# Kernel tuning notes

Measured on AMD Instinct MI355X. Metric: run time of the kernel, lower is better.

The kernel has to match this reference:

```python
import jax, jax.numpy as jnp
import numpy as np

N_CLASS = 32
SOS = 30
EOS = 31
NEG = -10000.0


def setup_inputs() -> dict:
    key = jax.random.key(0)
    k1, k2 = jax.random.split(key)
    seq_len, batch = 512, 2048
    feats = jax.random.normal(k1, (seq_len, batch, N_CLASS), dtype=jnp.float32)
    mask = jnp.ones((seq_len, batch), dtype=jnp.float32)
    transition = jax.random.normal(k2, (N_CLASS, N_CLASS), dtype=jnp.float32)
    # reset_parameters: transitions into <SOS> and out of <EOS> are forbidden
    transition = transition.at[SOS, :].set(NEG)
    transition = transition.at[:, EOS].set(NEG)
    return {"feats": feats, "mask": mask, "transition": transition}


def reference(feats, mask, transition):
    seq_len, batch, n_class = feats.shape
    alpha0 = jnp.full((batch, n_class), NEG, dtype=feats.dtype).at[:, SOS].set(0.0)

    def step(alpha, inp):
        feat, mask_t = inp  # feat: (B, C), mask_t: (B,)
        # scores[b, next, prev] = alpha[b, prev] + transition[next, prev] + feat[b, next]
        scores = alpha[:, None, :] + transition[None, :, :] + feat[:, :, None]
        new_alpha = jax.nn.logsumexp(scores, axis=-1)
        m = mask_t[:, None]
        alpha = new_alpha * m + alpha * (1.0 - m)
        return alpha, None

    alpha, _ = jax.lax.scan(step, alpha0, (feats, mask))
    alpha = alpha + transition[EOS][None, :]
    return jax.nn.logsumexp(alpha, axis=-1)  # (batch,)
```

## Files before the change

kernel.cpp:

```cpp
#include <hip/hip_runtime.h>

#define NCLS  32
#define SOS   30
#define EOS   31
#define LOG2E 1.4426950408889634f
#define LN2   0.6931471805599453f

typedef __attribute__((ext_vector_type(8))) short short8;
typedef __attribute__((ext_vector_type(4))) float f32x4;

__device__ __forceinline__ uint32_t rne_bf16(float x) {
    uint32_t u = __float_as_uint(x);
    return (u + 0x7fffu + ((u >> 16) & 1u)) >> 16;
}

__global__ __launch_bounds__(128, 2) void crf_fwd(const float* __restrict__ feats,
                                                  const float* __restrict__ mask,
                                                  const float* __restrict__ trans,
                                                  float* __restrict__ out,
                                                  int S, int B) {
    __shared__ float mxs[2][NCLS];
    __shared__ __align__(16) float wsh[2][NCLS];
    __shared__ float wsc[2];

    const int tid  = threadIdx.x;
    const int wid  = tid >> 6;
    const int lane = tid & 63;
    const int q  = lane >> 4;
    const int n0 = lane & 15;
    const int k0 = q * 8;
    const int b  = blockIdx.x * 2 + (n0 & 1);
    const int bb = (b < B) ? b : (B - 1);

    if (lane < NCLS) {
        float mx = -3.4e38f;
        #pragma unroll
        for (int k = 0; k < NCLS; ++k)
            mx = fmaxf(mx, wid ? trans[k * NCLS + lane] : trans[lane * NCLS + k]);
        mxs[wid][lane] = mx * LOG2E;
    }
    __builtin_amdgcn_wave_barrier();
    const float* mx_ = mxs[wid];

    const int c1 = ((n0 >> 2) << 3) | (n0 & 3);
    const int c2 = c1 + 4;
    const float nc1 = mx_[c1], nc2 = mx_[c2];
    union { uint32_t u[4]; short8 s; } a1u, a2u;
    #pragma unroll
    for (int j2 = 0; j2 < 4; ++j2) {
        const int ka = k0 + 2 * j2, kb = ka + 1;
        float f0 = __builtin_amdgcn_exp2f((wid ? trans[ka*NCLS + c1] : trans[c1*NCLS + ka]) * LOG2E - nc1);
        float f1 = __builtin_amdgcn_exp2f((wid ? trans[kb*NCLS + c1] : trans[c1*NCLS + kb]) * LOG2E - nc1);
        a1u.u[j2] = rne_bf16(f0) | (rne_bf16(f1) << 16);
        float g0 = __builtin_amdgcn_exp2f((wid ? trans[ka*NCLS + c2] : trans[c2*NCLS + ka]) * LOG2E - nc2);
        float g1 = __builtin_amdgcn_exp2f((wid ? trans[kb*NCLS + c2] : trans[c2*NCLS + kb]) * LOG2E - nc2);
        a2u.u[j2] = rne_bf16(g0) | (rne_bf16(g1) << 16);
    }
    const short8 a1 = a1u.s, a2 = a2u.s;

    const float mtAx = mx_[k0+0] - 6.f, mtAy = mx_[k0+1] - 6.f;
    const float mtAz = mx_[k0+2] - 6.f, mtAw = mx_[k0+3] - 6.f;
    const float mtBx = mx_[k0+4] - 6.f, mtBy = mx_[k0+5] - 6.f;
    const float mtBz = mx_[k0+6] - 6.f, mtBw = mx_[k0+7] - 6.f;

    float E1x = 0.f, E1y = 0.f, E1z = 0.f, E1w = 0.f;
    float E2x = 0.f, E2y = 0.f, E2z = 0.f, E2w = 0.f;
    if (wid == 0) {
        if (q == 3) E2z = 1.0f;
    } else {
        E1x = __builtin_amdgcn_exp2f(trans[EOS*NCLS + k0+0] * LOG2E - mx_[k0+0]);
        E1y = __builtin_amdgcn_exp2f(trans[EOS*NCLS + k0+1] * LOG2E - mx_[k0+1]);
        E1z = __builtin_amdgcn_exp2f(trans[EOS*NCLS + k0+2] * LOG2E - mx_[k0+2]);
        E1w = __builtin_amdgcn_exp2f(trans[EOS*NCLS + k0+3] * LOG2E - mx_[k0+3]);
        E2x = __builtin_amdgcn_exp2f(trans[EOS*NCLS + k0+4] * LOG2E - mx_[k0+4]);
        E2y = __builtin_amdgcn_exp2f(trans[EOS*NCLS + k0+5] * LOG2E - mx_[k0+5]);
        E2z = __builtin_amdgcn_exp2f(trans[EOS*NCLS + k0+6] * LOG2E - mx_[k0+6]);
        E2w = __builtin_amdgcn_exp2f(trans[EOS*NCLS + k0+7] * LOG2E - mx_[k0+7]);
    }
    float C = 0.f, cnt = 0.f;

    const long long fstep = (long long)B * NCLS;
    const int Hf = (S + 1) >> 1;
    const int H  = wid ? (S - Hf) : Hf;
    const int r0 = wid ? (S - 1) : 0;
    const long long dstep = wid ? -fstep : fstep;
    const long long mstep = wid ? -(long long)B : (long long)B;
    const float* fbase = feats + (long long)r0 * fstep + (long long)bb * NCLS + k0;
    const float* mbase = mask + (long long)r0 * B + bb;

#define LOADSLOT(Rf1, Rf2, Rm, T) {                                          \
        const float* _p = fbase + (long long)(T) * dstep;                    \
        Rf1 = *(const f32x4*)_p;                                             \
        Rf2 = *(const f32x4*)(_p + 4);                                       \
        Rm  = mbase[(long long)(T) * mstep];                                 \
    }

#define CONV(Rf1, Rf2, Rm, Ea, Eb, Md) {                                     \
        Ea.x = __builtin_amdgcn_exp2f(fmaf(Rf1.x, LOG2E, mtAx));             \
        Ea.y = __builtin_amdgcn_exp2f(fmaf(Rf1.y, LOG2E, mtAy));             \
        Ea.z = __builtin_amdgcn_exp2f(fmaf(Rf1.z, LOG2E, mtAz));             \
        Ea.w = __builtin_amdgcn_exp2f(fmaf(Rf1.w, LOG2E, mtAw));             \
        Eb.x = __builtin_amdgcn_exp2f(fmaf(Rf2.x, LOG2E, mtBx));             \
        Eb.y = __builtin_amdgcn_exp2f(fmaf(Rf2.y, LOG2E, mtBy));             \
        Eb.z = __builtin_amdgcn_exp2f(fmaf(Rf2.z, LOG2E, mtBz));             \
        Eb.w = __builtin_amdgcn_exp2f(fmaf(Rf2.w, LOG2E, mtBw));             \
        Md = Rm;                                                             \
    }

#define RENORM_E {                                                           \
        float _Dv = __shfl(E1x, n0, 64);          \
        uint32_t _eb = (__float_as_uint(_Dv) >> 23) & 0xffu;                 \
        C += (float)((int)_eb - 127);                                        \
        float _sc = __uint_as_float((254u - _eb) << 23);                     \
        E1x *= _sc; E1y *= _sc; E1z *= _sc; E1w *= _sc;                      \
        E2x *= _sc; E2y *= _sc; E2z *= _sc; E2w *= _sc;                      \
    }

#define STEPF(EFa, EFb, EM, RN) {                                            \
        uint32_t p0 = __builtin_amdgcn_perm(__float_as_uint(E1y), __float_as_uint(E1x), 0x07060302u); \
        uint32_t p1 = __builtin_amdgcn_perm(__float_as_uint(E1w), __float_as_uint(E1z), 0x07060302u); \
        uint32_t p2 = __builtin_amdgcn_perm(__float_as_uint(E2y), __float_as_uint(E2x), 0x07060302u); \
        uint32_t p3 = __builtin_amdgcn_perm(__float_as_uint(E2w), __float_as_uint(E2z), 0x07060302u); \
        union { uint32_t u[4]; short8 s; } _bu;                              \
        _bu.u[0] = p0; _bu.u[1] = p1; _bu.u[2] = p2; _bu.u[3] = p3;          \
        const f32x4 _z = {0.f, 0.f, 0.f, 0.f};                               \
        f32x4 _d1 = __builtin_amdgcn_mfma_f32_16x16x32_bf16(a1, _bu.s, _z, 0, 0, 0); \
        f32x4 _d2 = __builtin_amdgcn_mfma_f32_16x16x32_bf16(a2, _bu.s, _z, 0, 0, 0); \
        const bool _s = (EM != 0.0f);                                        \
        E1x = _s ? _d1[0] * EFa.x : E1x;  E1y = _s ? _d1[1] * EFa.y : E1y;   \
        E1z = _s ? _d1[2] * EFa.z : E1z;  E1w = _s ? _d1[3] * EFa.w : E1w;   \
        E2x = _s ? _d2[0] * EFb.x : E2x;  E2y = _s ? _d2[1] * EFb.y : E2y;   \
        E2z = _s ? _d2[2] * EFb.z : E2z;  E2w = _s ? _d2[3] * EFb.w : E2w;   \
        cnt += EM;                                                           \
        if (RN) RENORM_E                                                     \
    }

#define STEPB(EFa, EFb, EM, RN) {                                            \
        float t1x = E1x * EFa.x, t1y = E1y * EFa.y, t1z = E1z * EFa.z, t1w = E1w * EFa.w; \
        float t2x = E2x * EFb.x, t2y = E2y * EFb.y, t2z = E2z * EFb.z, t2w = E2w * EFb.w; \
        uint32_t p0 = __builtin_amdgcn_perm(__float_as_uint(t1y), __float_as_uint(t1x), 0x07060302u); \
        uint32_t p1 = __builtin_amdgcn_perm(__float_as_uint(t1w), __float_as_uint(t1z), 0x07060302u); \
        uint32_t p2 = __builtin_amdgcn_perm(__float_as_uint(t2y), __float_as_uint(t2x), 0x07060302u); \
        uint32_t p3 = __builtin_amdgcn_perm(__float_as_uint(t2w), __float_as_uint(t2z), 0x07060302u); \
        union { uint32_t u[4]; short8 s; } _bu;                              \
        _bu.u[0] = p0; _bu.u[1] = p1; _bu.u[2] = p2; _bu.u[3] = p3;          \
        const f32x4 _z = {0.f, 0.f, 0.f, 0.f};                               \
        f32x4 _d1 = __builtin_amdgcn_mfma_f32_16x16x32_bf16(a1, _bu.s, _z, 0, 0, 0); \
        f32x4 _d2 = __builtin_amdgcn_mfma_f32_16x16x32_bf16(a2, _bu.s, _z, 0, 0, 0); \
        const bool _s = (EM != 0.0f);                                        \
        E1x = _s ? _d1[0] : E1x;  E1y = _s ? _d1[1] : E1y;                   \
        E1z = _s ? _d1[2] : E1z;  E1w = _s ? _d1[3] : E1w;                   \
        E2x = _s ? _d2[0] : E2x;  E2y = _s ? _d2[1] : E2y;                   \
        E2z = _s ? _d2[2] : E2z;  E2w = _s ? _d2[3] : E2w;                   \
        cnt += EM;                                                           \
        if (RN) RENORM_E                                                     \
    }

#define PIPELINE(STEPM) {                                                    \
        f32x4 r1_0, r1_1, r1_2, r1_3, r2_0, r2_1, r2_2, r2_3;                \
        float rm_0, rm_1, rm_2, rm_3;                                        \
        f32x4 e1_0, e2_0, e1_1, e2_1;                                        \
        float m_0, m_1;                                                      \
        int tb = 0;                                                          \
        if (H >= 8) {                                                        \
            LOADSLOT(r1_0, r2_0, rm_0, 0); LOADSLOT(r1_1, r2_1, rm_1, 1);    \
            LOADSLOT(r1_2, r2_2, rm_2, 2); LOADSLOT(r1_3, r2_3, rm_3, 3);    \
            CONV(r1_0, r2_0, rm_0, e1_0, e2_0, m_0);                         \
            CONV(r1_1, r2_1, rm_1, e1_1, e2_1, m_1);                         \
            for (; tb + 8 <= H; tb += 4) {                                   \
                STEPM(e1_0, e2_0, m_0, false)                                \
                CONV(r1_2, r2_2, rm_2, e1_0, e2_0, m_0);                     \
                LOADSLOT(r1_0, r2_0, rm_0, tb + 4);                          \
                STEPM(e1_1, e2_1, m_1, false)                                \
                CONV(r1_3, r2_3, rm_3, e1_1, e2_1, m_1);                     \
                LOADSLOT(r1_1, r2_1, rm_1, tb + 5);                          \
                STEPM(e1_0, e2_0, m_0, false)                                \
                CONV(r1_0, r2_0, rm_0, e1_0, e2_0, m_0);                     \
                LOADSLOT(r1_2, r2_2, rm_2, tb + 6);                          \
                STEPM(e1_1, e2_1, m_1, true)                                 \
                CONV(r1_1, r2_1, rm_1, e1_1, e2_1, m_1);                     \
                LOADSLOT(r1_3, r2_3, rm_3, tb + 7);                          \
            }                                                                \
        }                                                                    \
        for (int t = tb; t < H; ++t) {         \
            f32x4 tf1, tf2; float tmr;                                       \
            LOADSLOT(tf1, tf2, tmr, t);                                      \
            f32x4 te1, te2; float tem;                                       \
            CONV(tf1, tf2, tmr, te1, te2, tem);                              \
            STEPM(te1, te2, tem, ((t & 3) == 3))                             \
        }                                                                    \
    }

    if (wid == 0) { PIPELINE(STEPF) } else { PIPELINE(STEPB) }

    if (wid == 1) {
        if (n0 < 2) {
            wsh[n0][k0+0] = E1x * __builtin_amdgcn_exp2f(mx_[k0+0]);
            wsh[n0][k0+1] = E1y * __builtin_amdgcn_exp2f(mx_[k0+1]);
            wsh[n0][k0+2] = E1z * __builtin_amdgcn_exp2f(mx_[k0+2]);
            wsh[n0][k0+3] = E1w * __builtin_amdgcn_exp2f(mx_[k0+3]);
            wsh[n0][k0+4] = E2x * __builtin_amdgcn_exp2f(mx_[k0+4]);
            wsh[n0][k0+5] = E2y * __builtin_amdgcn_exp2f(mx_[k0+5]);
            wsh[n0][k0+6] = E2z * __builtin_amdgcn_exp2f(mx_[k0+6]);
            wsh[n0][k0+7] = E2w * __builtin_amdgcn_exp2f(mx_[k0+7]);
            if (q == 0) wsc[n0] = C + 6.0f * cnt;
        }
    }
    __syncthreads();
    if (wid == 0) {
        const int bc = n0 & 1;
        const f32x4 wa = *(const f32x4*)&wsh[bc][k0];
        const f32x4 wb = *(const f32x4*)&wsh[bc][k0 + 4];
        float dot = E1x * wa.x + E1y * wa.y + E1z * wa.z + E1w * wa.w
                  + E2x * wb.x + E2y * wb.y + E2z * wb.z + E2w * wb.w;
        dot += __shfl_xor(dot, 16, 64);
        dot += __shfl_xor(dot, 32, 64);
        if (q == 0 && n0 < 2 && b < B) {
            out[b] = LN2 * (C + 6.0f * cnt + wsc[bc] + __builtin_amdgcn_logf(dot));
        }
    }
#undef LOADSLOT
#undef CONV
#undef RENORM_E
#undef STEPF
#undef STEPB
#undef PIPELINE
}

extern "C" void kernel_launch(void* const* d_in, const int* in_sizes, int n_in,
                              void* d_out, int out_size, void* d_ws, size_t ws_size,
                              hipStream_t stream) {
    const float* feats = (const float*)d_in[0];
    const float* mask  = (const float*)d_in[1];
    const float* trans = (const float*)d_in[2];
    float* out = (float*)d_out;

    const int B = out_size;
    const int S = in_sizes[1] / B;

    dim3 block(128);
    dim3 grid((B + 1) / 2);
    hipLaunchKernelGGL(crf_fwd, grid, block, 0, stream, feats, mask, trans, out, S, B);
}
```

Baseline: 226.2 us.

## Pack 16 batch columns per MFMA tile and deepen the load pipeline to 8 slots

Each block now handles 16 batch elements, one per MFMA N column, where it used to handle 2 that were replicated across the columns. The grid shrinks by a factor of 8. The prefetch ring grows from 4 to 8 timesteps with an explicit epilogue, and launch bounds drop to 1 block per CU so the extra registers fit. This removes redundant MFMA work and fixed per-block overhead, at the cost of fewer blocks (128 for B=2048) to cover the CUs and lower occupancy for hiding latency.

New measurement: 247.1 us. 9.2% more time.

```diff
diff --git a/kernel.cpp b/kernel.cpp
--- a/kernel.cpp
+++ b/kernel.cpp
@@ -14,14 +14,14 @@
     return (u + 0x7fffu + ((u >> 16) & 1u)) >> 16;
 }
 
-__global__ __launch_bounds__(128, 2) void crf_fwd(const float* __restrict__ feats,
+__global__ __launch_bounds__(128, 1) void crf_fwd(const float* __restrict__ feats,
                                                   const float* __restrict__ mask,
                                                   const float* __restrict__ trans,
                                                   float* __restrict__ out,
                                                   int S, int B) {
     __shared__ float mxs[2][NCLS];
-    __shared__ __align__(16) float wsh[2][NCLS];
-    __shared__ float wsc[2];
+    __shared__ __align__(16) float wsh[16][NCLS];
+    __shared__ float wsc[16];
 
     const int tid  = threadIdx.x;
     const int wid  = tid >> 6;
@@ -29,7 +29,7 @@
     const int q  = lane >> 4;
     const int n0 = lane & 15;
     const int k0 = q * 8;
-    const int b  = blockIdx.x * 2 + (n0 & 1);
+    const int b  = blockIdx.x * 16 + n0;
     const int bb = (b < B) ? b : (B - 1);
 
     if (lane < NCLS) {
@@ -108,7 +108,7 @@
     }
 
 #define RENORM_E {                                                           \
-        float _Dv = __shfl(E1x, n0, 64);          \
+        float _Dv = __shfl(E1x, n0, 64);         \
         uint32_t _eb = (__float_as_uint(_Dv) >> 23) & 0xffu;                 \
         C += (float)((int)_eb - 127);                                        \
         float _sc = __uint_as_float((254u - _eb) << 23);                     \
@@ -157,30 +157,61 @@
     }
 
 #define PIPELINE(STEPM) {                                                    \
-        f32x4 r1_0, r1_1, r1_2, r1_3, r2_0, r2_1, r2_2, r2_3;                \
-        float rm_0, rm_1, rm_2, rm_3;                                        \
+        f32x4 r1_0, r1_1, r1_2, r1_3, r1_4, r1_5, r1_6, r1_7;                \
+        f32x4 r2_0, r2_1, r2_2, r2_3, r2_4, r2_5, r2_6, r2_7;                \
+        float rm_0, rm_1, rm_2, rm_3, rm_4, rm_5, rm_6, rm_7;                \
         f32x4 e1_0, e2_0, e1_1, e2_1;                                        \
         float m_0, m_1;                                                      \
         int tb = 0;                                                          \
-        if (H >= 8) {                                                        \
+        if (H >= 16) {                                                       \
             LOADSLOT(r1_0, r2_0, rm_0, 0); LOADSLOT(r1_1, r2_1, rm_1, 1);    \
             LOADSLOT(r1_2, r2_2, rm_2, 2); LOADSLOT(r1_3, r2_3, rm_3, 3);    \
+            LOADSLOT(r1_4, r2_4, rm_4, 4); LOADSLOT(r1_5, r2_5, rm_5, 5);    \
+            LOADSLOT(r1_6, r2_6, rm_6, 6); LOADSLOT(r1_7, r2_7, rm_7, 7);    \
             CONV(r1_0, r2_0, rm_0, e1_0, e2_0, m_0);                         \
             CONV(r1_1, r2_1, rm_1, e1_1, e2_1, m_1);                         \
-            for (; tb + 8 <= H; tb += 4) {                                   \
+            for (; tb + 16 <= H; tb += 8) {                                  \
                 STEPM(e1_0, e2_0, m_0, false)                                \
                 CONV(r1_2, r2_2, rm_2, e1_0, e2_0, m_0);                     \
-                LOADSLOT(r1_0, r2_0, rm_0, tb + 4);                          \
+                LOADSLOT(r1_0, r2_0, rm_0, tb + 8);                          \
                 STEPM(e1_1, e2_1, m_1, false)                                \
                 CONV(r1_3, r2_3, rm_3, e1_1, e2_1, m_1);                     \
-                LOADSLOT(r1_1, r2_1, rm_1, tb + 5);                          \
+                LOADSLOT(r1_1, r2_1, rm_1, tb + 9);                          \
+                STEPM(e1_0, e2_0, m_0, false)                                \
+                CONV(r1_4, r2_4, rm_4, e1_0, e2_0, m_0);                     \
+                LOADSLOT(r1_2, r2_2, rm_2, tb + 10);                         \
+                STEPM(e1_1, e2_1, m_1, true)                                 \
+                CONV(r1_5, r2_5, rm_5, e1_1, e2_1, m_1);                     \
+                LOADSLOT(r1_3, r2_3, rm_3, tb + 11);                         \
+                STEPM(e1_0, e2_0, m_0, false)                                \
+                CONV(r1_6, r2_6, rm_6, e1_0, e2_0, m_0);                     \
+                LOADSLOT(r1_4, r2_4, rm_4, tb + 12);                         \
+                STEPM(e1_1, e2_1, m_1, false)                                \
+                CONV(r1_7, r2_7, rm_7, e1_1, e2_1, m_1);                     \
+                LOADSLOT(r1_5, r2_5, rm_5, tb + 13);                         \
                 STEPM(e1_0, e2_0, m_0, false)                                \
                 CONV(r1_0, r2_0, rm_0, e1_0, e2_0, m_0);                     \
-                LOADSLOT(r1_2, r2_2, rm_2, tb + 6);                          \
+                LOADSLOT(r1_6, r2_6, rm_6, tb + 14);                         \
                 STEPM(e1_1, e2_1, m_1, true)                                 \
                 CONV(r1_1, r2_1, rm_1, e1_1, e2_1, m_1);                     \
-                LOADSLOT(r1_3, r2_3, rm_3, tb + 7);                          \
+                LOADSLOT(r1_7, r2_7, rm_7, tb + 15);                         \
             }                                                                \
+               \
+            STEPM(e1_0, e2_0, m_0, false)                                    \
+            CONV(r1_2, r2_2, rm_2, e1_0, e2_0, m_0);                         \
+            STEPM(e1_1, e2_1, m_1, false)                                    \
+            CONV(r1_3, r2_3, rm_3, e1_1, e2_1, m_1);                         \
+            STEPM(e1_0, e2_0, m_0, false)                                    \
+            CONV(r1_4, r2_4, rm_4, e1_0, e2_0, m_0);                         \
+            STEPM(e1_1, e2_1, m_1, true)                                     \
+            CONV(r1_5, r2_5, rm_5, e1_1, e2_1, m_1);                         \
+            STEPM(e1_0, e2_0, m_0, false)                                    \
+            CONV(r1_6, r2_6, rm_6, e1_0, e2_0, m_0);                         \
+            STEPM(e1_1, e2_1, m_1, false)                                    \
+            CONV(r1_7, r2_7, rm_7, e1_1, e2_1, m_1);                         \
+            STEPM(e1_0, e2_0, m_0, false)                                    \
+            STEPM(e1_1, e2_1, m_1, true)                                     \
+            tb += 8;                                                         \
         }                                                                    \
         for (int t = tb; t < H; ++t) {         \
             f32x4 tf1, tf2; float tmr;                                       \
@@ -194,29 +225,26 @@
     if (wid == 0) { PIPELINE(STEPF) } else { PIPELINE(STEPB) }
 
     if (wid == 1) {
-        if (n0 < 2) {
-            wsh[n0][k0+0] = E1x * __builtin_amdgcn_exp2f(mx_[k0+0]);
-            wsh[n0][k0+1] = E1y * __builtin_amdgcn_exp2f(mx_[k0+1]);
-            wsh[n0][k0+2] = E1z * __builtin_amdgcn_exp2f(mx_[k0+2]);
-            wsh[n0][k0+3] = E1w * __builtin_amdgcn_exp2f(mx_[k0+3]);
-            wsh[n0][k0+4] = E2x * __builtin_amdgcn_exp2f(mx_[k0+4]);
-            wsh[n0][k0+5] = E2y * __builtin_amdgcn_exp2f(mx_[k0+5]);
-            wsh[n0][k0+6] = E2z * __builtin_amdgcn_exp2f(mx_[k0+6]);
-            wsh[n0][k0+7] = E2w * __builtin_amdgcn_exp2f(mx_[k0+7]);
-            if (q == 0) wsc[n0] = C + 6.0f * cnt;
-        }
+        wsh[n0][k0+0] = E1x * __builtin_amdgcn_exp2f(mx_[k0+0]);
+        wsh[n0][k0+1] = E1y * __builtin_amdgcn_exp2f(mx_[k0+1]);
+        wsh[n0][k0+2] = E1z * __builtin_amdgcn_exp2f(mx_[k0+2]);
+        wsh[n0][k0+3] = E1w * __builtin_amdgcn_exp2f(mx_[k0+3]);
+        wsh[n0][k0+4] = E2x * __builtin_amdgcn_exp2f(mx_[k0+4]);
+        wsh[n0][k0+5] = E2y * __builtin_amdgcn_exp2f(mx_[k0+5]);
+        wsh[n0][k0+6] = E2z * __builtin_amdgcn_exp2f(mx_[k0+6]);
+        wsh[n0][k0+7] = E2w * __builtin_amdgcn_exp2f(mx_[k0+7]);
+        if (q == 0) wsc[n0] = C + 6.0f * cnt;
     }
     __syncthreads();
     if (wid == 0) {
-        const int bc = n0 & 1;
-        const f32x4 wa = *(const f32x4*)&wsh[bc][k0];
-        const f32x4 wb = *(const f32x4*)&wsh[bc][k0 + 4];
+        const f32x4 wa = *(const f32x4*)&wsh[n0][k0];
+        const f32x4 wb = *(const f32x4*)&wsh[n0][k0 + 4];
         float dot = E1x * wa.x + E1y * wa.y + E1z * wa.z + E1w * wa.w
                   + E2x * wb.x + E2y * wb.y + E2z * wb.z + E2w * wb.w;
         dot += __shfl_xor(dot, 16, 64);
         dot += __shfl_xor(dot, 32, 64);
-        if (q == 0 && n0 < 2 && b < B) {
-            out[b] = LN2 * (C + 6.0f * cnt + wsc[bc] + __builtin_amdgcn_logf(dot));
+        if (q == 0 && b < B) {
+            out[b] = LN2 * (C + 6.0f * cnt + wsc[n0] + __builtin_amdgcn_logf(dot));
         }
     }
 #undef LOADSLOT
@@ -239,6 +267,6 @@
     const int S = in_sizes[1] / B;
 
     dim3 block(128);
-    dim3 grid((B + 1) / 2);
+    dim3 grid((B + 15) / 16);
     hipLaunchKernelGGL(crf_fwd, grid, block, 0, stream, feats, mask, trans, out, S, B);
 }
```

## Stage feats and mask through a deep LDS ring via direct global-to-LDS loads

Applied to the files above, without the earlier changes.

Each block now handles 16 batch rows instead of 2, with every MFMA column holding a distinct sequence. Per-step feats and mask slices are prefetched with global_load_lds into a 16-deep per-wave LDS ring, gated by explicit vmcnt waits. The aim is to keep many loads in flight to hide global latency in the serial recurrence and to stop wasting MFMA columns on duplicate batches. In exchange the grid shrinks 8x (128 blocks), occupancy drops to one block per CU with large LDS use, and correctness relies on hand-tuned vmcnt counts.

Result: slower. 313.6 us (+38.6%).

```diff
diff --git a/kernel.cpp b/kernel.cpp
--- a/kernel.cpp
+++ b/kernel.cpp
@@ -6,6 +6,10 @@
 #define LOG2E 1.4426950408889634f
 #define LN2   0.6931471805599453f
 
+#define RING_D  16
+#define SLOT_B  2304
+#define RING_B  (RING_D * SLOT_B)
+
 typedef __attribute__((ext_vector_type(8))) short short8;
 typedef __attribute__((ext_vector_type(4))) float f32x4;
 
@@ -14,14 +18,27 @@
     return (u + 0x7fffu + ((u >> 16) & 1u)) >> 16;
 }
 
-__global__ __launch_bounds__(128, 2) void crf_fwd(const float* __restrict__ feats,
+__device__ __forceinline__ void dma16(const float* g, char* l) {
+    __builtin_amdgcn_global_load_lds((const __attribute__((address_space(1))) void*)g,
+                                     (__attribute__((address_space(3))) void*)l, 16, 0, 0);
+}
+__device__ __forceinline__ void dma4(const float* g, char* l) {
+    __builtin_amdgcn_global_load_lds((const __attribute__((address_space(1))) void*)g,
+                                     (__attribute__((address_space(3))) void*)l, 4, 0, 0);
+}
+
+#define WAITV45 asm volatile("s_waitcnt vmcnt(45)" ::: "memory")
+#define WAITV42 asm volatile("s_waitcnt vmcnt(42)" ::: "memory")
+
+__global__ __launch_bounds__(128, 1) void crf_fwd(const float* __restrict__ feats,
                                                   const float* __restrict__ mask,
                                                   const float* __restrict__ trans,
                                                   float* __restrict__ out,
                                                   int S, int B) {
     __shared__ float mxs[2][NCLS];
-    __shared__ __align__(16) float wsh[2][NCLS];
-    __shared__ float wsc[2];
+    __shared__ __align__(16) float wsh[16][NCLS];
+    __shared__ float wsc[16];
+    __shared__ __align__(16) char ring[2][RING_B];
 
     const int tid  = threadIdx.x;
     const int wid  = tid >> 6;
@@ -29,8 +46,11 @@
     const int q  = lane >> 4;
     const int n0 = lane & 15;
     const int k0 = q * 8;
-    const int b  = blockIdx.x * 2 + (n0 & 1);
+    const int b  = blockIdx.x * 16 + n0;
     const int bb = (b < B) ? b : (B - 1);
+    const int l16 = lane << 4;
+    const int l4  = lane << 2;
+    char* const slotbase = &ring[wid][0];
 
     if (lane < NCLS) {
         float mx = -3.4e38f;
@@ -88,11 +108,20 @@
     const float* fbase = feats + (long long)r0 * fstep + (long long)bb * NCLS + k0;
     const float* mbase = mask + (long long)r0 * B + bb;
 
-#define LOADSLOT(Rf1, Rf2, Rm, T) {                                          \
-        const float* _p = fbase + (long long)(T) * dstep;                    \
-        Rf1 = *(const f32x4*)_p;                                             \
-        Rf2 = *(const f32x4*)(_p + 4);                                       \
-        Rm  = mbase[(long long)(T) * mstep];                                 \
+#define STAGE(TS, SLOT) {                                                    \
+        const float* _gf = fbase + (long long)(TS) * dstep;                  \
+        const float* _gm = mbase + (long long)(TS) * mstep;                  \
+        char* _l = slotbase + (SLOT) * SLOT_B;                               \
+        dma16(_gf,     _l);                                                  \
+        dma16(_gf + 4, _l + 1024);                                           \
+        dma4 (_gm,     _l + 2048);                                           \
+    }
+
+#define READSLOT(SLOT, Rf1, Rf2, Rm) {                                       \
+        const char* _l = slotbase + (SLOT) * SLOT_B;                         \
+        Rf1 = *(const f32x4*)(_l + l16);                                     \
+        Rf2 = *(const f32x4*)(_l + 1024 + l16);                              \
+        Rm  = *(const float*)(_l + 2048 + l4);                               \
     }
 
 #define CONV(Rf1, Rf2, Rm, Ea, Eb, Md) {                                     \
@@ -108,7 +137,7 @@
     }
 
 #define RENORM_E {                                                           \
-        float _Dv = __shfl(E1x, n0, 64);          \
+        float _Dv = __shfl(E1x, n0, 64);         \
         uint32_t _eb = (__float_as_uint(_Dv) >> 23) & 0xffu;                 \
         C += (float)((int)_eb - 127);                                        \
         float _sc = __uint_as_float((254u - _eb) << 23);                     \
@@ -156,74 +185,84 @@
         if (RN) RENORM_E                                                     \
     }
 
+#define PIPEITER(T, U1, U2, Um, F1, F2, Fm, RN, STEPM) {                     \
+        { const int _ts = ((T) + RING_D - 1 < H) ? ((T) + RING_D - 1) : (H - 1); \
+          STAGE(_ts, ((T) - 1) & (RING_D - 1)) }                             \
+        WAITV42;                                                             \
+        { const int _tr = ((T) + 1 < H) ? ((T) + 1) : (H - 1);               \
+          READSLOT(_tr & (RING_D - 1), F1, F2, Fm) }                         \
+        STEPM(e1, e2, em, RN)                                                \
+        CONV(U1, U2, Um, e1, e2, em);                                        \
+    }
+
 #define PIPELINE(STEPM) {                                                    \
-        f32x4 r1_0, r1_1, r1_2, r1_3, r2_0, r2_1, r2_2, r2_3;                \
-        float rm_0, rm_1, rm_2, rm_3;                                        \
-        f32x4 e1_0, e2_0, e1_1, e2_1;                                        \
-        float m_0, m_1;                                                      \
-        int tb = 0;                                                          \
-        if (H >= 8) {                                                        \
-            LOADSLOT(r1_0, r2_0, rm_0, 0); LOADSLOT(r1_1, r2_1, rm_1, 1);    \
-            LOADSLOT(r1_2, r2_2, rm_2, 2); LOADSLOT(r1_3, r2_3, rm_3, 3);    \
-            CONV(r1_0, r2_0, rm_0, e1_0, e2_0, m_0);                         \
-            CONV(r1_1, r2_1, rm_1, e1_1, e2_1, m_1);                         \
-            for (; tb + 8 <= H; tb += 4) {                                   \
-                STEPM(e1_0, e2_0, m_0, false)                                \
-                CONV(r1_2, r2_2, rm_2, e1_0, e2_0, m_0);                     \
-                LOADSLOT(r1_0, r2_0, rm_0, tb + 4);                          \
-                STEPM(e1_1, e2_1, m_1, false)                                \
-                CONV(r1_3, r2_3, rm_3, e1_1, e2_1, m_1);                     \
-                LOADSLOT(r1_1, r2_1, rm_1, tb + 5);                          \
-                STEPM(e1_0, e2_0, m_0, false)                                \
-                CONV(r1_0, r2_0, rm_0, e1_0, e2_0, m_0);                     \
-                LOADSLOT(r1_2, r2_2, rm_2, tb + 6);                          \
-                STEPM(e1_1, e2_1, m_1, true)                                 \
-                CONV(r1_1, r2_1, rm_1, e1_1, e2_1, m_1);                     \
-                LOADSLOT(r1_3, r2_3, rm_3, tb + 7);                          \
-            }                                                                \
+        f32x4 e1, e2; float em;                                              \
+        f32x4 rA1, rA2, rB1, rB2; float rAm, rBm;                            \
+               \
+        _Pragma("unroll")                                                    \
+        for (int s = 0; s < RING_D; ++s) {                                   \
+            const int _ps = (s < H) ? s : (H - 1);                           \
+            STAGE(_ps, s)                                                    \
         }                                                                    \
-        for (int t = tb; t < H; ++t) {         \
-            f32x4 tf1, tf2; float tmr;                                       \
-            LOADSLOT(tf1, tf2, tmr, t);                                      \
-            f32x4 te1, te2; float tem;                                       \
-            CONV(tf1, tf2, tmr, te1, te2, tem);                              \
-            STEPM(te1, te2, tem, ((t & 3) == 3))                             \
+        WAITV45;                                          \
+        READSLOT(0, rA1, rA2, rAm)                                           \
+        WAITV42;                                          \
+        { const int _t1 = (1 < H) ? 1 : 0;                                   \
+          READSLOT(_t1, rB1, rB2, rBm) }                                     \
+        CONV(rA1, rA2, rAm, e1, e2, em);                                     \
+        int t = 1;                                                           \
+        for (; t + 3 < H; t += 4) {                                          \
+            PIPEITER(t+0, rB1, rB2, rBm, rA1, rA2, rAm, false, STEPM)        \
+            PIPEITER(t+1, rA1, rA2, rAm, rB1, rB2, rBm, false, STEPM)        \
+            PIPEITER(t+2, rB1, rB2, rBm, rA1, rA2, rAm, false, STEPM)        \
+            PIPEITER(t+3, rA1, rA2, rAm, rB1, rB2, rBm, true,  STEPM)        \
         }                                                                    \
-    }
-
-    if (wid == 0) { PIPELINE(STEPF) } else { PIPELINE(STEPB) }
+        for (; t < H; ++t) {              \
+            { const int _ts = (t + RING_D - 1 < H) ? (t + RING_D - 1) : (H - 1); \
+              STAGE(_ts, (t - 1) & (RING_D - 1)) }                           \
+            WAITV42;                                                         \
+            f32x4 x1, x2; float xm;                                          \
+            READSLOT(t & (RING_D - 1), x1, x2, xm)                           \
+            STEPM(e1, e2, em, true)                                          \
+            CONV(x1, x2, xm, e1, e2, em);                                    \
+        }                                                                    \
+        STEPM(e1, e2, em, true)                    \
+    }
+
+    if (H > 0) {
+        if (wid == 0) { PIPELINE(STEPF) } else { PIPELINE(STEPB) }
+    }
 
     if (wid == 1) {
-        if (n0 < 2) {
-            wsh[n0][k0+0] = E1x * __builtin_amdgcn_exp2f(mx_[k0+0]);
-            wsh[n0][k0+1] = E1y * __builtin_amdgcn_exp2f(mx_[k0+1]);
-            wsh[n0][k0+2] = E1z * __builtin_amdgcn_exp2f(mx_[k0+2]);
-            wsh[n0][k0+3] = E1w * __builtin_amdgcn_exp2f(mx_[k0+3]);
-            wsh[n0][k0+4] = E2x * __builtin_amdgcn_exp2f(mx_[k0+4]);
-            wsh[n0][k0+5] = E2y * __builtin_amdgcn_exp2f(mx_[k0+5]);
-            wsh[n0][k0+6] = E2z * __builtin_amdgcn_exp2f(mx_[k0+6]);
-            wsh[n0][k0+7] = E2w * __builtin_amdgcn_exp2f(mx_[k0+7]);
-            if (q == 0) wsc[n0] = C + 6.0f * cnt;
-        }
+        wsh[n0][k0+0] = E1x * __builtin_amdgcn_exp2f(mx_[k0+0]);
+        wsh[n0][k0+1] = E1y * __builtin_amdgcn_exp2f(mx_[k0+1]);
+        wsh[n0][k0+2] = E1z * __builtin_amdgcn_exp2f(mx_[k0+2]);
+        wsh[n0][k0+3] = E1w * __builtin_amdgcn_exp2f(mx_[k0+3]);
+        wsh[n0][k0+4] = E2x * __builtin_amdgcn_exp2f(mx_[k0+4]);
+        wsh[n0][k0+5] = E2y * __builtin_amdgcn_exp2f(mx_[k0+5]);
+        wsh[n0][k0+6] = E2z * __builtin_amdgcn_exp2f(mx_[k0+6]);
+        wsh[n0][k0+7] = E2w * __builtin_amdgcn_exp2f(mx_[k0+7]);
+        if (q == 0) wsc[n0] = C + 6.0f * cnt;
     }
     __syncthreads();
     if (wid == 0) {
-        const int bc = n0 & 1;
-        const f32x4 wa = *(const f32x4*)&wsh[bc][k0];
-        const f32x4 wb = *(const f32x4*)&wsh[bc][k0 + 4];
+        const f32x4 wa = *(const f32x4*)&wsh[n0][k0];
+        const f32x4 wb = *(const f32x4*)&wsh[n0][k0 + 4];
         float dot = E1x * wa.x + E1y * wa.y + E1z * wa.z + E1w * wa.w
                   + E2x * wb.x + E2y * wb.y + E2z * wb.z + E2w * wb.w;
         dot += __shfl_xor(dot, 16, 64);
         dot += __shfl_xor(dot, 32, 64);
-        if (q == 0 && n0 < 2 && b < B) {
-            out[b] = LN2 * (C + 6.0f * cnt + wsc[bc] + __builtin_amdgcn_logf(dot));
+        if (q == 0 && b < B) {
+            out[b] = LN2 * (C + 6.0f * cnt + wsc[n0] + __builtin_amdgcn_logf(dot));
         }
     }
-#undef LOADSLOT
+#undef STAGE
+#undef READSLOT
 #undef CONV
 #undef RENORM_E
 #undef STEPF
 #undef STEPB
+#undef PIPEITER
 #undef PIPELINE
 }
 
@@ -239,6 +278,6 @@
     const int S = in_sizes[1] / B;
 
     dim3 block(128);
-    dim3 grid((B + 1) / 2);
+    dim3 grid((B + 15) / 16);
     hipLaunchKernelGGL(crf_fwd, grid, block, 0, stream, feats, mask, trans, out, S, B);
 }
```

## Pack 16 sequences per MFMA wave and deepen asm-driven load pipeline to 8 stages

Applied to the files above, without the earlier changes.

Each wave now processes 16 batch elements in the MFMA N dimension instead of 2 duplicated ones, cutting the grid 8x and removing redundant work. Feature loads are issued via inline asm global_load with explicit vmcnt waits and an 8-deep prefetch ring to hide memory latency on the serial recurrence. The launch bound drops to 1 block per SM minimum to allow more registers for the ring. Risks include lower occupancy (128 blocks on many CUs) and 32-bit offsets that could overflow for larger inputs.

After: 193.7 us. 14.4% less time.

```diff
diff --git a/kernel.cpp b/kernel.cpp
--- a/kernel.cpp
+++ b/kernel.cpp
@@ -14,14 +14,14 @@
     return (u + 0x7fffu + ((u >> 16) & 1u)) >> 16;
 }
 
-__global__ __launch_bounds__(128, 2) void crf_fwd(const float* __restrict__ feats,
+__global__ __launch_bounds__(128, 1) void crf_fwd(const float* __restrict__ feats,
                                                   const float* __restrict__ mask,
                                                   const float* __restrict__ trans,
                                                   float* __restrict__ out,
                                                   int S, int B) {
     __shared__ float mxs[2][NCLS];
-    __shared__ __align__(16) float wsh[2][NCLS];
-    __shared__ float wsc[2];
+    __shared__ __align__(16) float wsh[16][NCLS];
+    __shared__ float wsc[16];
 
     const int tid  = threadIdx.x;
     const int wid  = tid >> 6;
@@ -29,7 +29,7 @@
     const int q  = lane >> 4;
     const int n0 = lane & 15;
     const int k0 = q * 8;
-    const int b  = blockIdx.x * 2 + (n0 & 1);
+    const int b  = blockIdx.x * 16 + n0;
     const int bb = (b < B) ? b : (B - 1);
 
     if (lane < NCLS) {
@@ -85,15 +85,26 @@
     const int r0 = wid ? (S - 1) : 0;
     const long long dstep = wid ? -fstep : fstep;
     const long long mstep = wid ? -(long long)B : (long long)B;
-    const float* fbase = feats + (long long)r0 * fstep + (long long)bb * NCLS + k0;
-    const float* mbase = mask + (long long)r0 * B + bb;
-
-#define LOADSLOT(Rf1, Rf2, Rm, T) {                                          \
-        const float* _p = fbase + (long long)(T) * dstep;                    \
-        Rf1 = *(const f32x4*)_p;                                             \
-        Rf2 = *(const f32x4*)(_p + 4);                                       \
-        Rm  = mbase[(long long)(T) * mstep];                                 \
-    }
+    const int Hm1 = H - 1;
+    const uint32_t dstepB = (uint32_t)(int)(dstep * 4);
+    const uint32_t mstepB = (uint32_t)(int)(mstep * 4);
+    uint32_t vofF = (uint32_t)(((long long)r0 * fstep + (long long)bb * NCLS + k0) * 4);
+    uint32_t vofM = (uint32_t)(((long long)r0 * B + bb) * 4);
+
+    f32x4 sf1_0, sf1_1, sf1_2, sf1_3, sf1_4, sf1_5, sf1_6, sf1_7;
+    f32x4 sf2_0, sf2_1, sf2_2, sf2_3, sf2_4, sf2_5, sf2_6, sf2_7;
+    float sm_0, sm_1, sm_2, sm_3, sm_4, sm_5, sm_6, sm_7;
+
+#define ISSUE3(k, OF, OM)                                                    \
+    asm volatile("global_load_dwordx4 %0, %3, %4\n\t"                        \
+                 "global_load_dwordx4 %1, %3, %4 offset:16\n\t"              \
+                 "global_load_dword %2, %5, %6"                              \
+                 : "=&v"(sf1_##k), "=&v"(sf2_##k), "=&v"(sm_##k)             \
+                 : "v"(OF), "s"(feats), "v"(OM), "s"(mask)                   \
+                 : "memory");
+
+#define WAITV21 { asm volatile("s_waitcnt vmcnt(21)" ::: "memory");          \
+                  __builtin_amdgcn_sched_barrier(0); }
 
 #define CONV(Rf1, Rf2, Rm, Ea, Eb, Md) {                                     \
         Ea.x = __builtin_amdgcn_exp2f(fmaf(Rf1.x, LOG2E, mtAx));             \
@@ -108,7 +119,7 @@
     }
 
 #define RENORM_E {                                                           \
-        float _Dv = __shfl(E1x, n0, 64);          \
+        float _Dv = __shfl(E1x, n0, 64);         \
         uint32_t _eb = (__float_as_uint(_Dv) >> 23) & 0xffu;                 \
         C += (float)((int)_eb - 127);                                        \
         float _sc = __uint_as_float((254u - _eb) << 23);                     \
@@ -156,74 +167,85 @@
         if (RN) RENORM_E                                                     \
     }
 
+#define GSTEP(k, RN, STEPM) {                                                \
+        WAITV21                                                              \
+        f32x4 e1, e2; float em;                                              \
+        CONV(sf1_##k, sf2_##k, sm_##k, e1, e2, em);                          \
+        STEPM(e1, e2, em, RN)                                                \
+        ISSUE3(k, pfF, pfM)                                                  \
+        { const uint32_t _a = (stageT < Hm1) ? 1u : 0u;                      \
+          pfF += _a ? dstepB : 0u;                                           \
+          pfM += _a ? mstepB : 0u;                                           \
+          stageT += (int)_a; }                                               \
+    }
+
+#define TSTEP(k, VMC, STEPM)                                                 \
+    if (t + k < H) {                                                         \
+        asm volatile("s_waitcnt vmcnt(" #VMC ")" ::: "memory");              \
+        __builtin_amdgcn_sched_barrier(0);                                   \
+        f32x4 e1, e2; float em;                                              \
+        CONV(sf1_##k, sf2_##k, sm_##k, e1, e2, em);                          \
+        STEPM(e1, e2, em, true)                                              \
+    }
+
+#define PROI(k) ISSUE3(k, oF, oM)                                            \
+    if (k < Hm1) { oF += dstepB; oM += mstepB; }
+
 #define PIPELINE(STEPM) {                                                    \
-        f32x4 r1_0, r1_1, r1_2, r1_3, r2_0, r2_1, r2_2, r2_3;                \
-        float rm_0, rm_1, rm_2, rm_3;                                        \
-        f32x4 e1_0, e2_0, e1_1, e2_1;                                        \
-        float m_0, m_1;                                                      \
-        int tb = 0;                                                          \
-        if (H >= 8) {                                                        \
-            LOADSLOT(r1_0, r2_0, rm_0, 0); LOADSLOT(r1_1, r2_1, rm_1, 1);    \
-            LOADSLOT(r1_2, r2_2, rm_2, 2); LOADSLOT(r1_3, r2_3, rm_3, 3);    \
-            CONV(r1_0, r2_0, rm_0, e1_0, e2_0, m_0);                         \
-            CONV(r1_1, r2_1, rm_1, e1_1, e2_1, m_1);                         \
-            for (; tb + 8 <= H; tb += 4) {                                   \
-                STEPM(e1_0, e2_0, m_0, false)                                \
-                CONV(r1_2, r2_2, rm_2, e1_0, e2_0, m_0);                     \
-                LOADSLOT(r1_0, r2_0, rm_0, tb + 4);                          \
-                STEPM(e1_1, e2_1, m_1, false)                                \
-                CONV(r1_3, r2_3, rm_3, e1_1, e2_1, m_1);                     \
-                LOADSLOT(r1_1, r2_1, rm_1, tb + 5);                          \
-                STEPM(e1_0, e2_0, m_0, false)                                \
-                CONV(r1_0, r2_0, rm_0, e1_0, e2_0, m_0);                     \
-                LOADSLOT(r1_2, r2_2, rm_2, tb + 6);                          \
-                STEPM(e1_1, e2_1, m_1, true)                                 \
-                CONV(r1_1, r2_1, rm_1, e1_1, e2_1, m_1);                     \
-                LOADSLOT(r1_3, r2_3, rm_3, tb + 7);                          \
-            }                                                                \
+        uint32_t oF = vofF, oM = vofM;                                       \
+        PROI(0) PROI(1) PROI(2) PROI(3) PROI(4) PROI(5) PROI(6) PROI(7)      \
+        uint32_t pfF = oF, pfM = oM;                                         \
+        int stageT = (Hm1 < 8) ? Hm1 : 8;                                    \
+        int t = 0;                                                           \
+        for (; t + 8 <= H; t += 8) {                                         \
+            GSTEP(0, false, STEPM) GSTEP(1, false, STEPM)                    \
+            GSTEP(2, false, STEPM) GSTEP(3, true,  STEPM)                    \
+            GSTEP(4, false, STEPM) GSTEP(5, false, STEPM)                    \
+            GSTEP(6, false, STEPM) GSTEP(7, true,  STEPM)                    \
         }                                                                    \
-        for (int t = tb; t < H; ++t) {         \
-            f32x4 tf1, tf2; float tmr;                                       \
-            LOADSLOT(tf1, tf2, tmr, t);                                      \
-            f32x4 te1, te2; float tem;                                       \
-            CONV(tf1, tf2, tmr, te1, te2, tem);                              \
-            STEPM(te1, te2, tem, ((t & 3) == 3))                             \
-        }                                                                    \
-    }
-
-    if (wid == 0) { PIPELINE(STEPF) } else { PIPELINE(STEPB) }
+        TSTEP(0, 21, STEPM) TSTEP(1, 18, STEPM) TSTEP(2, 15, STEPM)          \
+        TSTEP(3, 12, STEPM) TSTEP(4, 9,  STEPM) TSTEP(5, 6,  STEPM)          \
+        TSTEP(6, 3,  STEPM)                                                  \
+        asm volatile("s_waitcnt vmcnt(0)" ::: "memory");                     \
+        __builtin_amdgcn_sched_barrier(0);                                   \
+    }
+
+    if (H > 0) {
+        if (wid == 0) { PIPELINE(STEPF) } else { PIPELINE(STEPB) }
+    }
 
     if (wid == 1) {
-        if (n0 < 2) {
-            wsh[n0][k0+0] = E1x * __builtin_amdgcn_exp2f(mx_[k0+0]);
-            wsh[n0][k0+1] = E1y * __builtin_amdgcn_exp2f(mx_[k0+1]);
-            wsh[n0][k0+2] = E1z * __builtin_amdgcn_exp2f(mx_[k0+2]);
-            wsh[n0][k0+3] = E1w * __builtin_amdgcn_exp2f(mx_[k0+3]);
-            wsh[n0][k0+4] = E2x * __builtin_amdgcn_exp2f(mx_[k0+4]);
-            wsh[n0][k0+5] = E2y * __builtin_amdgcn_exp2f(mx_[k0+5]);
-            wsh[n0][k0+6] = E2z * __builtin_amdgcn_exp2f(mx_[k0+6]);
-            wsh[n0][k0+7] = E2w * __builtin_amdgcn_exp2f(mx_[k0+7]);
-            if (q == 0) wsc[n0] = C + 6.0f * cnt;
-        }
+        wsh[n0][k0+0] = E1x * __builtin_amdgcn_exp2f(mx_[k0+0]);
+        wsh[n0][k0+1] = E1y * __builtin_amdgcn_exp2f(mx_[k0+1]);
+        wsh[n0][k0+2] = E1z * __builtin_amdgcn_exp2f(mx_[k0+2]);
+        wsh[n0][k0+3] = E1w * __builtin_amdgcn_exp2f(mx_[k0+3]);
+        wsh[n0][k0+4] = E2x * __builtin_amdgcn_exp2f(mx_[k0+4]);
+        wsh[n0][k0+5] = E2y * __builtin_amdgcn_exp2f(mx_[k0+5]);
+        wsh[n0][k0+6] = E2z * __builtin_amdgcn_exp2f(mx_[k0+6]);
+        wsh[n0][k0+7] = E2w * __builtin_amdgcn_exp2f(mx_[k0+7]);
+        if (q == 0) wsc[n0] = C + 6.0f * cnt;
     }
     __syncthreads();
     if (wid == 0) {
-        const int bc = n0 & 1;
-        const f32x4 wa = *(const f32x4*)&wsh[bc][k0];
-        const f32x4 wb = *(const f32x4*)&wsh[bc][k0 + 4];
+        const f32x4 wa = *(const f32x4*)&wsh[n0][k0];
+        const f32x4 wb = *(const f32x4*)&wsh[n0][k0 + 4];
         float dot = E1x * wa.x + E1y * wa.y + E1z * wa.z + E1w * wa.w
                   + E2x * wb.x + E2y * wb.y + E2z * wb.z + E2w * wb.w;
         dot += __shfl_xor(dot, 16, 64);
         dot += __shfl_xor(dot, 32, 64);
-        if (q == 0 && n0 < 2 && b < B) {
-            out[b] = LN2 * (C + 6.0f * cnt + wsc[bc] + __builtin_amdgcn_logf(dot));
+        if (q == 0 && b < B) {
+            out[b] = LN2 * (C + 6.0f * cnt + wsc[n0] + __builtin_amdgcn_logf(dot));
         }
     }
-#undef LOADSLOT
+#undef ISSUE3
+#undef WAITV21
 #undef CONV
 #undef RENORM_E
 #undef STEPF
 #undef STEPB
+#undef GSTEP
+#undef TSTEP
+#undef PROI
 #undef PIPELINE
 }
 
@@ -239,6 +261,6 @@
     const int S = in_sizes[1] / B;
 
     dim3 block(128);
-    dim3 grid((B + 1) / 2);
+    dim3 grid((B + 15) / 16);
     hipLaunchKernelGGL(crf_fwd, grid, block, 0, stream, feats, mask, trans, out, S, B);
 }
```
